# Optimization experiments

Hardware: AMD Instinct MI355X
Metric: run time of the kernel (lower is better)

Reference implementation:

```python
import jax, jax.numpy as jnp
import numpy as np

LMAX = 8
RES_BETA = 32   # Gauss-Legendre points in beta (>= 2*LMAX+1 -> exact quadrature for product)
RES_ALPHA = 63  # uniform points in alpha (>= 2*(2*LMAX)+1)
BATCH = 16384
DIM = (LMAX + 1) ** 2  # 81 real SH coefficients, flat index i = l*l + l + m


def _normalized_assoc_legendre(lmax, y):
    # P[b, l, m] = orthonormalized associated Legendre \bar{P}_l^m(y), 0<=m<=l,
    # normalized so that int_{-1}^{1} Pbar_l^m Pbar_l'^m dy = delta_{ll'} / (2*pi).
    n = len(y)
    P = np.zeros((n, lmax + 1, lmax + 1))
    sx = np.sqrt(np.clip(1.0 - y * y, 0.0, None))
    P[:, 0, 0] = np.sqrt(1.0 / (4.0 * np.pi))
    for m in range(1, lmax + 1):
        P[:, m, m] = -np.sqrt((2.0 * m + 1.0) / (2.0 * m)) * sx * P[:, m - 1, m - 1]
    for m in range(lmax):
        P[:, m + 1, m] = np.sqrt(2.0 * m + 3.0) * y * P[:, m, m]
    for m in range(lmax + 1):
        for l in range(m + 2, lmax + 1):
            a = np.sqrt((4.0 * l * l - 1.0) / (l * l - m * m))
            b = np.sqrt(((l - 1.0) ** 2 - m * m) / (4.0 * (l - 1.0) ** 2 - 1.0))
            P[:, l, m] = a * (y * P[:, l - 1, m] - b * P[:, l - 2, m])
    return P


def _s2grid_basis():
    # Gauss-Legendre nodes y=cos(beta) and weights (integrate sin(beta) d(beta) exactly)
    y, w = np.polynomial.legendre.leggauss(RES_BETA)
    P = _normalized_assoc_legendre(LMAX, y)
    alphas = 2.0 * np.pi * np.arange(RES_ALPHA) / RES_ALPHA
    shb = np.zeros((RES_BETA, DIM))   # Legendre part, per flat (l,m) index
    sha = np.zeros((RES_ALPHA, DIM))  # Fourier part, per flat (l,m) index
    s2 = np.sqrt(2.0)
    for l in range(LMAX + 1):
        for m in range(-l, l + 1):
            i = l * l + l + m
            shb[:, i] = P[:, l, abs(m)]
            if m == 0:
                sha[:, i] = 1.0
            elif m > 0:
                sha[:, i] = s2 * np.cos(m * alphas)
            else:
                sha[:, i] = s2 * np.sin(-m * alphas)
    qw = w * (2.0 * np.pi / RES_ALPHA)  # combined beta quadrature + alpha trapezoid weight
    return (shb.astype(np.float32), sha.astype(np.float32), qw.astype(np.float32))


def setup_inputs() -> dict:
    key = jax.random.key(0)
    k1, k2 = jax.random.split(key)
    shb, sha, qw = _s2grid_basis()
    return {
        "input1": jax.random.normal(k1, (BATCH, DIM), dtype=jnp.float32),
        "input2": jax.random.normal(k2, (BATCH, DIM), dtype=jnp.float32),
        "shb": jnp.asarray(shb),
        "sha": jnp.asarray(sha),
        "qw": jnp.asarray(qw),
    }


def _to_s2grid(x, shb, sha):
    # x: [Z, D] -> grid: [Z, res_beta, res_alpha]
    t = jnp.einsum('zi,bi->zbi', x, shb)        # Legendre expansion along beta
    return jnp.einsum('zbi,ai->zba', t, sha)    # Fourier synthesis along alpha


def _from_s2grid(g, shb, sha, qw):
    # g: [Z, res_beta, res_alpha] -> coeffs: [Z, D]
    t = jnp.einsum('zba,ai->zbi', g, sha)       # Fourier analysis along alpha
    return jnp.einsum('zbi,bi,b->zi', t, shb, qw)  # Legendre projection with quadrature


def reference(input1, input2, shb, sha, qw):
    g1 = _to_s2grid(input1, shb, sha)
    g2 = _to_s2grid(input2, shb, sha)
    return _from_s2grid(g1 * g2, shb, sha, qw)
```

## Files before the change

kernel.cpp:

```cpp
#include <hip/hip_runtime.h>

#define DIM 81
#define RA  63
#define RB  32
#define ZT  32
#define XS  104
#define OS  100

#define OFF_SHAA 0
#define OFF_SHAT 12288
#define OFF_SHBH 24576
#define OFF_SHBQ 30720
#define WS_NEED  43008

#define LDS_TBL   18432
#define LDS_BYTES (18432 + 25600)

typedef _Float16 half8 __attribute__((ext_vector_type(8)));
typedef _Float16 half4v __attribute__((ext_vector_type(4)));
typedef __fp16  fp16x2 __attribute__((ext_vector_type(2)));
typedef float floatx16 __attribute__((ext_vector_type(16)));

union H8U { unsigned u[4]; half8 h; };
union H2U { fp16x2 h; unsigned u; };

__global__ __launch_bounds__(256) void precompute_fact(
    const float* __restrict__ shb, const float* __restrict__ sha,
    const float* __restrict__ qw, char* __restrict__ wsp)
{
    _Float16* shaAP = (_Float16*)(wsp + OFF_SHAA);
    _Float16* shaTP = (_Float16*)(wsp + OFF_SHAT);
    _Float16* shbHP = (_Float16*)(wsp + OFF_SHBH);
    float*    shbqP = (float*)(wsp + OFF_SHBQ);

    int idx = blockIdx.x * 256 + threadIdx.x;
    if (idx < 6144) {
        int j = idx & 7, lane = (idx >> 3) & 63, g = idx >> 9;
        int at = g / 6, kk = g - at * 6;
        int a = at * 32 + (lane & 31);
        int i = kk * 16 + (lane >> 5) * 8 + j;
        float v = (a < RA && i < DIM) ? sha[a * DIM + i] : 0.f;
        shaAP[idx] = (_Float16)v;
    } else if (idx < 12288) {
        int t = idx - 6144;
        int j = t & 7, lane = (t >> 3) & 63, g = t >> 9;
        int it = g >> 2, ks = g & 3;
        int a = ks * 16 + (lane >> 5) * 8 + j;
        int i = it * 32 + (lane & 31);
        float v = (a < RA && i < DIM) ? sha[a * DIM + i] : 0.f;
        shaTP[t] = (_Float16)v;
    } else if (idx < 15360) {
        int t = idx - 12288;
        int j = t & 7, hi = (t >> 3) & 1, g = t >> 4;
        int b = g / 6, kk = g - b * 6;
        int i = kk * 16 + hi * 8 + j;
        float v = (i < DIM) ? shb[b * DIM + i] : 0.f;
        shbHP[t] = (_Float16)v;
    } else if (idx < 18432) {
        int t = idx - 15360;
        int l = t & 31, g = t >> 5;
        int b = g / 3, it = g - b * 3;
        int i = it * 32 + l;
        float v = (i < DIM) ? shb[b * DIM + i] * qw[b] : 0.f;
        shbqP[t] = v;
    }
}

__global__ __launch_bounds__(256, 1) void gaunt_fact(
    const float* __restrict__ x1, const float* __restrict__ x2,
    const char* __restrict__ wsp, float* __restrict__ out)
{
    const _Float16* shaAP = (const _Float16*)(wsp + OFF_SHAA);
    const _Float16* shaTP = (const _Float16*)(wsp + OFF_SHAT);

    __shared__ __align__(16) char lds[LDS_BYTES];
    const _Float16* shbH_l = (const _Float16*)lds;
    const float*    shbq_l = (const float*)(lds + 6144);
    _Float16* xp = (_Float16*)(lds + LDS_TBL);
    float*    ob = (float*)(lds + LDS_TBL);

    const int tid = threadIdx.x;
    const int z0  = blockIdx.x * ZT;

    for (int i = tid; i < LDS_TBL / 16; i += 256)
        ((uint4*)lds)[i] = ((const uint4*)(wsp + OFF_SHBH))[i];

    {
        const int nv = ZT * 24;
        #pragma unroll
        for (int in = 0; in < 2; ++in) {
            const float* src = in ? x2 : x1;
            _Float16* dst = xp + in * (ZT * XS);
            for (int idx = tid; idx < nv; idx += 256) {
                int r = idx / 24, c4 = idx - r * 24;
                float4 v = make_float4(0.f, 0.f, 0.f, 0.f);
                if (c4 < 20)       v = *(const float4*)(src + (size_t)(z0 + r) * DIM + c4 * 4);
                else if (c4 == 20) v.x = src[(size_t)(z0 + r) * DIM + 80];
                half4v h;
                h[0] = (_Float16)v.x; h[1] = (_Float16)v.y;
                h[2] = (_Float16)v.z; h[3] = (_Float16)v.w;
                *(half4v*)(dst + r * XS + c4 * 4) = h;
            }
        }
    }
    __syncthreads();

    const int l = tid & 63, l31 = l & 31, hi = l >> 5;
    const int nw = tid >> 6;

    half8 xfr[2][6];
    #pragma unroll
    for (int in = 0; in < 2; ++in)
        #pragma unroll
        for (int kk = 0; kk < 6; ++kk)
            xfr[in][kk] = *(const half8*)(xp + in * (ZT * XS) + l31 * XS + kk * 16 + hi * 8);
    __syncthreads();

    half8 aAc[2][6];
    #pragma unroll
    for (int at = 0; at < 2; ++at)
        #pragma unroll
        for (int kk = 0; kk < 6; ++kk)
            aAc[at][kk] = *(const half8*)(shaAP + ((at * 6 + kk) * 64 + l) * 8);

    half8 bTc[3][2][2];
    #pragma unroll
    for (int it = 0; it < 3; ++it)
        #pragma unroll
        for (int at = 0; at < 2; ++at) {
            bTc[it][at][0] = *(const half8*)(shaTP + ((it * 4 + at * 2) * 64 + l) * 8);
            bTc[it][at][1] = *(const half8*)(shaTP + ((it * 4 + at * 2 + 1) * 64 + l) * 8);
        }

    floatx16 accO[3];
    #pragma unroll
    for (int it = 0; it < 3; ++it)
        #pragma unroll
        for (int r = 0; r < 16; ++r) accO[it][r] = 0.f;

    auto compute_f = [&](int b, unsigned fO[2][8]) {
        #pragma unroll
        for (int at = 0; at < 2; ++at) {
            floatx16 g0, g1;
            #pragma unroll
            for (int r = 0; r < 16; ++r) { g0[r] = 0.f; g1[r] = 0.f; }
            __builtin_amdgcn_s_setprio(1);
            #pragma unroll
            for (int kk = 0; kk < 6; ++kk) {
                const half8 sf = *(const half8*)(shbH_l + ((b * 6 + kk) * 2 + hi) * 8);
                const half8 aS = aAc[at][kk] * sf;
                g0 = __builtin_amdgcn_mfma_f32_32x32x16_f16(aS, xfr[0][kk], g0, 0, 0, 0);
                g1 = __builtin_amdgcn_mfma_f32_32x32x16_f16(aS, xfr[1][kk], g1, 0, 0, 0);
            }
            __builtin_amdgcn_s_setprio(0);
            floatx16 p = g0 * g1;
            unsigned q[8];
            #pragma unroll
            for (int j = 0; j < 8; ++j) {
                H2U t;
                t.h = __builtin_amdgcn_cvt_pkrtz(p[2 * j], p[2 * j + 1]);
                q[j] = t.u;
            }
            asm volatile("v_permlane32_swap_b32 %0, %1" : "+v"(q[0]), "+v"(q[2]));
            asm volatile("v_permlane32_swap_b32 %0, %1" : "+v"(q[1]), "+v"(q[3]));
            asm volatile("v_permlane32_swap_b32 %0, %1" : "+v"(q[4]), "+v"(q[6]));
            asm volatile("v_permlane32_swap_b32 %0, %1" : "+v"(q[5]), "+v"(q[7]));
            #pragma unroll
            for (int w = 0; w < 8; ++w) fO[at][w] = q[w];
        }
    };

    auto gemm2_acc = [&](int b, const unsigned fI[2][8]) {
        const float s0 = shbq_l[(b * 3 + 0) * 32 + l31];
        const float s1 = shbq_l[(b * 3 + 1) * 32 + l31];
        const float s2 = shbq_l[(b * 3 + 2) * 32 + l31];
        #pragma unroll
        for (int it = 0; it < 3; ++it) {
            floatx16 R;
            #pragma unroll
            for (int r = 0; r < 16; ++r) R[r] = 0.f;
            __builtin_amdgcn_s_setprio(1);
            #pragma unroll
            for (int at = 0; at < 2; ++at) {
                H8U a0, a1;
                a0.u[0] = fI[at][0]; a0.u[1] = fI[at][1]; a0.u[2] = fI[at][2]; a0.u[3] = fI[at][3];
                a1.u[0] = fI[at][4]; a1.u[1] = fI[at][5]; a1.u[2] = fI[at][6]; a1.u[3] = fI[at][7];
                R = __builtin_amdgcn_mfma_f32_32x32x16_f16(a0.h, bTc[it][at][0], R, 0, 0, 0);
                R = __builtin_amdgcn_mfma_f32_32x32x16_f16(a1.h, bTc[it][at][1], R, 0, 0, 0);
            }
            __builtin_amdgcn_s_setprio(0);
            const float s = (it == 0) ? s0 : (it == 1) ? s1 : s2;
            accO[it] += R * s;
        }
    };

    unsigned fc[2][8], fn[2][8];
    compute_f(nw * 8, fc);
    #pragma unroll 1
    for (int bi = 0; bi < 7; ++bi) {
        compute_f(nw * 8 + bi + 1, fn);
        gemm2_acc(nw * 8 + bi, fc);
        #pragma unroll
        for (int at = 0; at < 2; ++at)
            #pragma unroll
            for (int w = 0; w < 8; ++w) fc[at][w] = fn[at][w];
    }
    gemm2_acc(nw * 8 + 7, fc);

    if (nw >= 2) {
        float* buf = ob + (nw - 2) * (ZT * OS);
        #pragma unroll
        for (int it = 0; it < 3; ++it)
            #pragma unroll
            for (int r = 0; r < 16; ++r)
                buf[((r & 3) + 8 * (r >> 2) + 4 * hi) * OS + it * 32 + l31] = accO[it][r];
    }
    __syncthreads();
    if (nw < 2) {
        float* buf = ob + nw * (ZT * OS);
        #pragma unroll
        for (int it = 0; it < 3; ++it)
            #pragma unroll
            for (int r = 0; r < 16; ++r)
                accO[it][r] += buf[((r & 3) + 8 * (r >> 2) + 4 * hi) * OS + it * 32 + l31];
    }
    __syncthreads();
    if (nw < 2) {
        float* buf = ob + nw * (ZT * OS);
        #pragma unroll
        for (int it = 0; it < 3; ++it)
            #pragma unroll
            for (int r = 0; r < 16; ++r)
                buf[((r & 3) + 8 * (r >> 2) + 4 * hi) * OS + it * 32 + l31] = accO[it][r];
    }
    __syncthreads();

    for (int idx = tid; idx < ZT * DIM; idx += 256) {
        int zz = idx / DIM, ii = idx - zz * DIM;
        out[(size_t)z0 * DIM + idx] = ob[zz * OS + ii] + ob[ZT * OS + zz * OS + ii];
    }
}

__device__ __forceinline__ float wave_sum64(float v) {
    v += __int_as_float(__builtin_amdgcn_update_dpp(0, __float_as_int(v), 0x111, 0xf, 0xf, true));
    v += __int_as_float(__builtin_amdgcn_update_dpp(0, __float_as_int(v), 0x112, 0xf, 0xf, true));
    v += __int_as_float(__builtin_amdgcn_update_dpp(0, __float_as_int(v), 0x114, 0xf, 0xf, true));
    v += __int_as_float(__builtin_amdgcn_update_dpp(0, __float_as_int(v), 0x118, 0xf, 0xf, true));
    v += __int_as_float(__builtin_amdgcn_update_dpp(0, __float_as_int(v), 0x142, 0xf, 0xf, true));
    v += __int_as_float(__builtin_amdgcn_update_dpp(0, __float_as_int(v), 0x143, 0xf, 0xf, true));
    return v;
}

__global__ __launch_bounds__(256) void gaunt_s2grid_kernel(
    const float* __restrict__ x1, const float* __restrict__ x2,
    const float* __restrict__ shb, const float* __restrict__ sha,
    const float* __restrict__ qw, float* __restrict__ out)
{
    __shared__ float sha_s[64 * DIM];
    __shared__ float part[4 * DIM];
    const int tid = threadIdx.x;
    const int z = blockIdx.x;
    for (int idx = tid; idx < 64 * DIM; idx += 256)
        sha_s[idx] = (idx < RA * DIM) ? sha[idx] : 0.0f;
    __syncthreads();
    const int lane = tid & 63;
    const int w = __builtin_amdgcn_readfirstlane(tid >> 6);
    const int b0 = w * 8;
    const float* xz1 = x1 + (size_t)z * DIM;
    const float* xz2 = x2 + (size_t)z * DIM;
    const float* sha_row = sha_s + lane * DIM;
    float g1[8], g2[8];
    #pragma unroll
    for (int bb = 0; bb < 8; ++bb) { g1[bb] = 0.0f; g2[bb] = 0.0f; }
    #pragma unroll 4
    for (int i = 0; i < DIM; ++i) {
        const float sv = sha_row[i];
        const float t1 = xz1[i] * sv, t2 = xz2[i] * sv;
        #pragma unroll
        for (int bb = 0; bb < 8; ++bb) {
            const float h = shb[(b0 + bb) * DIM + i];
            g1[bb] = fmaf(h, t1, g1[bb]);
            g2[bb] = fmaf(h, t2, g2[bb]);
        }
    }
    float q[8];
    #pragma unroll
    for (int bb = 0; bb < 8; ++bb) q[bb] = g1[bb] * g2[bb] * qw[b0 + bb];
    #pragma unroll 4
    for (int i = 0; i < DIM; ++i) {
        float t = 0.0f;
        #pragma unroll
        for (int bb = 0; bb < 8; ++bb) t = fmaf(q[bb], shb[(b0 + bb) * DIM + i], t);
        float v = wave_sum64(t * sha_row[i]);
        if (lane == 63) part[w * DIM + i] = v;
    }
    __syncthreads();
    for (int i = tid; i < DIM; i += 256)
        out[(size_t)z * DIM + i] = part[i] + part[DIM + i] + part[2 * DIM + i] + part[3 * DIM + i];
}

extern "C" void kernel_launch(void* const* d_in, const int* in_sizes, int n_in,
                              void* d_out, int out_size, void* d_ws, size_t ws_size,
                              hipStream_t stream) {
    const float* x1  = (const float*)d_in[0];
    const float* x2  = (const float*)d_in[1];
    const float* shb = (const float*)d_in[2];
    const float* sha = (const float*)d_in[3];
    const float* qw  = (const float*)d_in[4];
    float* out = (float*)d_out;

    const int Z = in_sizes[0] / DIM;

    if (ws_size >= WS_NEED && (Z % ZT) == 0) {
        char* wsp = (char*)d_ws;
        precompute_fact<<<72, 256, 0, stream>>>(shb, sha, qw, wsp);
        gaunt_fact<<<Z / ZT, 256, 0, stream>>>(x1, x2, wsp, out);
    } else {
        gaunt_s2grid_kernel<<<Z, 256, 0, stream>>>(x1, x2, shb, sha, qw, out);
    }
}
```

Baseline: 39.27 us.

## Drop software pipelining of beta loop and split MFMA accumulation chains

Replaces the software-pipelined loop, which computed the next beta row's grid product while running the projection GEMM for the current one, with a plain sequential loop over beta rows. To recover instruction-level parallelism inside each row, the K reduction of the synthesis MFMAs is split into two independent accumulator chains that are summed before the product. This frees the registers held by the double-buffered fragments and cuts the dependent MFMA chain length. The cost is losing overlap between the two GEMM stages and adding extra accumulator registers and vector adds.

```diff
diff --git a/kernel.cpp b/kernel.cpp
--- a/kernel.cpp
+++ b/kernel.cpp
@@ -138,22 +138,34 @@
         #pragma unroll
         for (int r = 0; r < 16; ++r) accO[it][r] = 0.f;
 
-    auto compute_f = [&](int b, unsigned fO[2][8]) {
+    #pragma unroll 1
+    for (int bi = 0; bi < 8; ++bi) {
+        const int b = nw * 8 + bi;
+
+        unsigned f[2][8];
+
         #pragma unroll
         for (int at = 0; at < 2; ++at) {
-            floatx16 g0, g1;
-            #pragma unroll
-            for (int r = 0; r < 16; ++r) { g0[r] = 0.f; g1[r] = 0.f; }
+            floatx16 g0a, g0b, g1a, g1b;
+            #pragma unroll
+            for (int r = 0; r < 16; ++r) { g0a[r] = 0.f; g0b[r] = 0.f; g1a[r] = 0.f; g1b[r] = 0.f; }
             __builtin_amdgcn_s_setprio(1);
             #pragma unroll
-            for (int kk = 0; kk < 6; ++kk) {
+            for (int kk = 0; kk < 3; ++kk) {
                 const half8 sf = *(const half8*)(shbH_l + ((b * 6 + kk) * 2 + hi) * 8);
                 const half8 aS = aAc[at][kk] * sf;
-                g0 = __builtin_amdgcn_mfma_f32_32x32x16_f16(aS, xfr[0][kk], g0, 0, 0, 0);
-                g1 = __builtin_amdgcn_mfma_f32_32x32x16_f16(aS, xfr[1][kk], g1, 0, 0, 0);
+                g0a = __builtin_amdgcn_mfma_f32_32x32x16_f16(aS, xfr[0][kk], g0a, 0, 0, 0);
+                g1a = __builtin_amdgcn_mfma_f32_32x32x16_f16(aS, xfr[1][kk], g1a, 0, 0, 0);
+            }
+            #pragma unroll
+            for (int kk = 3; kk < 6; ++kk) {
+                const half8 sf = *(const half8*)(shbH_l + ((b * 6 + kk) * 2 + hi) * 8);
+                const half8 aS = aAc[at][kk] * sf;
+                g0b = __builtin_amdgcn_mfma_f32_32x32x16_f16(aS, xfr[0][kk], g0b, 0, 0, 0);
+                g1b = __builtin_amdgcn_mfma_f32_32x32x16_f16(aS, xfr[1][kk], g1b, 0, 0, 0);
             }
             __builtin_amdgcn_s_setprio(0);
-            floatx16 p = g0 * g1;
+            floatx16 p = (g0a + g0b) * (g1a + g1b);
             unsigned q[8];
             #pragma unroll
             for (int j = 0; j < 8; ++j) {
@@ -166,11 +178,9 @@
             asm volatile("v_permlane32_swap_b32 %0, %1" : "+v"(q[4]), "+v"(q[6]));
             asm volatile("v_permlane32_swap_b32 %0, %1" : "+v"(q[5]), "+v"(q[7]));
             #pragma unroll
-            for (int w = 0; w < 8; ++w) fO[at][w] = q[w];
-        }
-    };
-
-    auto gemm2_acc = [&](int b, const unsigned fI[2][8]) {
+            for (int w = 0; w < 8; ++w) f[at][w] = q[w];
+        }
+
         const float s0 = shbq_l[(b * 3 + 0) * 32 + l31];
         const float s1 = shbq_l[(b * 3 + 1) * 32 + l31];
         const float s2 = shbq_l[(b * 3 + 2) * 32 + l31];
@@ -183,8 +193,8 @@
             #pragma unroll
             for (int at = 0; at < 2; ++at) {
                 H8U a0, a1;
-                a0.u[0] = fI[at][0]; a0.u[1] = fI[at][1]; a0.u[2] = fI[at][2]; a0.u[3] = fI[at][3];
-                a1.u[0] = fI[at][4]; a1.u[1] = fI[at][5]; a1.u[2] = fI[at][6]; a1.u[3] = fI[at][7];
+                a0.u[0] = f[at][0]; a0.u[1] = f[at][1]; a0.u[2] = f[at][2]; a0.u[3] = f[at][3];
+                a1.u[0] = f[at][4]; a1.u[1] = f[at][5]; a1.u[2] = f[at][6]; a1.u[3] = f[at][7];
                 R = __builtin_amdgcn_mfma_f32_32x32x16_f16(a0.h, bTc[it][at][0], R, 0, 0, 0);
                 R = __builtin_amdgcn_mfma_f32_32x32x16_f16(a1.h, bTc[it][at][1], R, 0, 0, 0);
             }
@@ -192,20 +202,7 @@
             const float s = (it == 0) ? s0 : (it == 1) ? s1 : s2;
             accO[it] += R * s;
         }
-    };
-
-    unsigned fc[2][8], fn[2][8];
-    compute_f(nw * 8, fc);
-    #pragma unroll 1
-    for (int bi = 0; bi < 7; ++bi) {
-        compute_f(nw * 8 + bi + 1, fn);
-        gemm2_acc(nw * 8 + bi, fc);
-        #pragma unroll
-        for (int at = 0; at < 2; ++at)
-            #pragma unroll
-            for (int w = 0; w < 8; ++w) fc[at][w] = fn[at][w];
-    }
-    gemm2_acc(nw * 8 + 7, fc);
+    }
 
     if (nw >= 2) {
         float* buf = ob + (nw - 2) * (ZT * OS);
```

Result: slower. 41.81 us (+6.5%).
